# Kernel optimization log

Hardware: AMD Instinct MI355X
Metric: run time of the kernel (lower is better)

The kernel has to match this reference:

```python
import jax, jax.numpy as jnp
import numpy as np

N = 50_000       # nodes
E = 1_600_000    # edges (avg degree 32)
F_IN = 128       # input features
H = 32           # hidden channels (both GCNConv layers)
C = 16           # num classes


def setup_inputs() -> dict:
    key = jax.random.key(0)
    ks = jax.random.split(key, 6)
    x = jax.random.normal(ks[0], (N, F_IN), dtype=jnp.float32)
    edge_index = jax.random.randint(ks[1], (2, E), 0, N, dtype=jnp.int32)
    W1 = jax.random.normal(ks[2], (F_IN, H), dtype=jnp.float32) / np.float32(np.sqrt(F_IN))
    b1 = jnp.zeros((H,), jnp.float32)
    W2 = jax.random.normal(ks[3], (H, H), dtype=jnp.float32) / np.float32(np.sqrt(H))
    b2 = jnp.zeros((H,), jnp.float32)
    Wc = jax.random.normal(ks[4], (H, C), dtype=jnp.float32) / np.float32(np.sqrt(H))
    bc = jnp.zeros((C,), jnp.float32)
    return {"x": x, "edge_index": edge_index, "W1": W1, "b1": b1,
            "W2": W2, "b2": b2, "Wc": Wc, "bc": bc}


def _gcn_conv(x, W, b, src, dst, deg_inv_sqrt, n):
    """PyG GCNConv: xW, then D^{-1/2}(A+I)D^{-1/2} aggregation, then bias.

    src/dst already include self-loops; deg_inv_sqrt precomputed on dst.
    """
    xw = x @ W                                   # [N, H]
    norm = deg_inv_sqrt[src] * deg_inv_sqrt[dst]  # [E+N]
    msg = xw[src] * norm[:, None]                # gather + scale, [E+N, H]
    out = jax.ops.segment_sum(msg, dst, num_segments=n)  # scatter-add
    return out + b


def reference(x, edge_index, W1, b1, W2, b2, Wc, bc):
    n = x.shape[0]
    loops = jnp.arange(n, dtype=edge_index.dtype)
    src = jnp.concatenate([edge_index[0], loops])  # add self-loops
    dst = jnp.concatenate([edge_index[1], loops])
    # degree over destination column (edge weight 1), as PyG gcn_norm does
    deg = jax.ops.segment_sum(jnp.ones_like(dst, dtype=x.dtype), dst, num_segments=n)
    deg_inv_sqrt = jnp.where(deg > 0, jax.lax.rsqrt(deg), 0.0)

    h = jnp.tanh(_gcn_conv(x, W1, b1, src, dst, deg_inv_sqrt, n))
    h = jnp.tanh(_gcn_conv(h, W2, b2, src, dst, deg_inv_sqrt, n))
    out = h @ Wc + bc
    return (out, h)
```

## Files before the change

kernel.cpp:

```cpp
#include <hip/hip_runtime.h>
#include <hip/hip_bf16.h>

#define NN 50000
#define EE 1600000
#define FIN 128
#define HH 32
#define CC 16
#define NB 782
#define NBLK 391
#define CHUNK 4096

typedef unsigned short u16;
typedef unsigned int u32;
typedef unsigned char u8;

__device__ __forceinline__ float bf2f(u16 u) {
    union { u32 i; float f; } v; v.i = ((u32)u) << 16; return v.f;
}
__device__ __forceinline__ u16 f2bf(float f) {
    union { float f; u32 i; } v; v.f = f;
    u32 x = v.i;
    return (u16)((x + 0x7fffu + ((x >> 16) & 1u)) >> 16);
}

__global__ __launch_bounds__(256) void k_probe(const u32* __restrict__ xw_words, int* __restrict__ flag) {
    __shared__ int cs;
    if (threadIdx.x == 0) cs = 0;
    __syncthreads();
    int c = 0;
    for (int i = threadIdx.x; i < 512; i += 256) {
        float v = fabsf(bf2f((u16)(xw_words[i] & 0xffffu)));
        if (v >= 6.0e-8f && v <= 64.0f) c++;
    }
    atomicAdd(&cs, c);
    __syncthreads();
    if (threadIdx.x == 0) *flag = (cs > 384) ? 1 : 0;
}

__global__ __launch_bounds__(256) void k_place(const int* __restrict__ src, const int* __restrict__ dst,
                                               int* __restrict__ locT,
                                               u16* __restrict__ gsrc, u8* __restrict__ grel) {
    __shared__ int dst_s[CHUNK];
    __shared__ u16 s_src[CHUNK];
    __shared__ u8  s_rel[CHUNK];
    __shared__ int cur[NB];
    __shared__ int ps[256];
    const int tid = threadIdx.x, blk = blockIdx.x;
    const int e0 = blk * CHUNK;
    int cnt = EE - e0; if (cnt > CHUNK) cnt = CHUNK;

    const uint4* gd4 = (const uint4*)(dst + e0);
    for (int i = tid; i < cnt / 4; i += 256) ((uint4*)dst_s)[i] = gd4[i];
    for (int i = tid; i < NB; i += 256) cur[i] = 0;
    __syncthreads();

    for (int k = 0; k < CHUNK / 256; ++k) {
        int i = k * 256 + tid;
        if (i < cnt) atomicAdd(&cur[dst_s[i] >> 6], 1);
    }
    __syncthreads();

    const int bi = tid * 4;
    int v0 = 0, v1 = 0, v2 = 0, v3 = 0;
    if (bi < NB)     v0 = cur[bi];
    if (bi + 1 < NB) v1 = cur[bi + 1];
    if (bi + 2 < NB) v2 = cur[bi + 2];
    if (bi + 3 < NB) v3 = cur[bi + 3];
    ps[tid] = v0 + v1 + v2 + v3;
    __syncthreads();
    for (int off = 1; off < 256; off <<= 1) {
        int t = (tid >= off) ? ps[tid - off] : 0;
        __syncthreads();
        ps[tid] += t;
        __syncthreads();
    }
    int run = (tid == 0) ? 0 : ps[tid - 1];
    if (bi < NB)     { cur[bi] = run;     locT[(size_t)bi * NBLK + blk] = run;     run += v0; }
    if (bi + 1 < NB) { cur[bi + 1] = run; locT[(size_t)(bi + 1) * NBLK + blk] = run; run += v1; }
    if (bi + 2 < NB) { cur[bi + 2] = run; locT[(size_t)(bi + 2) * NBLK + blk] = run; run += v2; }
    if (bi + 3 < NB) { cur[bi + 3] = run; locT[(size_t)(bi + 3) * NBLK + blk] = run; run += v3; }
    if (tid == 255) locT[(size_t)NB * NBLK + blk] = ps[255];
    __syncthreads();

    for (int k = 0; k < CHUNK / 256; ++k) {
        int i = k * 256 + tid;
        if (i < cnt) {
            int d = dst_s[i];
            int pos = atomicAdd(&cur[d >> 6], 1);
            s_src[pos] = (u16)src[e0 + i];
            s_rel[pos] = (u8)(d & 63);
        }
    }
    __syncthreads();

    const uint4* ss = (const uint4*)s_src;
    uint4* gs = (uint4*)(gsrc + (size_t)blk * CHUNK);
    for (int i = tid; i < (cnt * 2) / 16; i += 256) gs[i] = ss[i];
    const uint4* sr = (const uint4*)s_rel;
    uint4* gr = (uint4*)(grel + (size_t)blk * CHUNK);
    for (int i = tid; i < cnt / 16; i += 256) gr[i] = sr[i];
}

__global__ __launch_bounds__(256) void k_btot(const int* __restrict__ locT, int* __restrict__ btot) {
    __shared__ int ps[256];
    const int cb = blockIdx.x;
    int s = 0;
    for (int b = threadIdx.x; b < NBLK; b += 256)
        s += locT[(size_t)(cb + 1) * NBLK + b] - locT[(size_t)cb * NBLK + b];
    ps[threadIdx.x] = s;
    __syncthreads();
    for (int off = 128; off > 0; off >>= 1) {
        if (threadIdx.x < off) ps[threadIdx.x] += ps[threadIdx.x + off];
        __syncthreads();
    }
    if (threadIdx.x == 0) btot[cb] = ps[0];
}

__global__ __launch_bounds__(1024) void k_cscan(const int* __restrict__ btot, int* __restrict__ cbase,
                                                int* __restrict__ rowptr) {
    __shared__ int ps[1024];
    const int t = threadIdx.x;
    int myv = (t < NB) ? btot[t] : 0;
    ps[t] = myv;
    __syncthreads();
    for (int off = 1; off < 1024; off <<= 1) {
        int v = (t >= off) ? ps[t - off] : 0;
        __syncthreads();
        ps[t] += v;
        __syncthreads();
    }
    if (t < NB) cbase[t] = ps[t] - myv;
    if (t == 0) { cbase[NB] = EE; rowptr[NN] = EE; }
}

__global__ __launch_bounds__(256) void k_fine(const int* __restrict__ locT, const int* __restrict__ cbase,
                                              const u16* __restrict__ gsrc, const u8* __restrict__ grel,
                                              int* __restrict__ rowptr, float* __restrict__ dis,
                                              u16* __restrict__ entries) {
    __shared__ int beg_s[NBLK];
    __shared__ int fo[NBLK + 1];
    __shared__ int ps[256];
    __shared__ int h[64];
    __shared__ int cur[64];
    const int tid = threadIdx.x, cb = blockIdx.x;

    for (int b = tid; b < NBLK; b += 256) {
        int beg = locT[(size_t)cb * NBLK + b];
        beg_s[b] = beg;
        fo[b] = locT[(size_t)(cb + 1) * NBLK + b] - beg;
    }
    if (tid < 64) h[tid] = 0;
    __syncthreads();

    const int b0 = tid * 2;
    int a = (b0 < NBLK) ? fo[b0] : 0;
    int b1v = (b0 + 1 < NBLK) ? fo[b0 + 1] : 0;
    ps[tid] = a + b1v;
    __syncthreads();
    for (int off = 1; off < 256; off <<= 1) {
        int v = (tid >= off) ? ps[tid - off] : 0;
        __syncthreads();
        ps[tid] += v;
        __syncthreads();
    }
    int run = (tid == 0) ? 0 : ps[tid - 1];
    if (b0 < NBLK)     { fo[b0] = run;     run += a; }
    if (b0 + 1 < NBLK) { fo[b0 + 1] = run; run += b1v; }
    if (tid == 255) fo[NBLK] = ps[255];
    __syncthreads();
    const int T = fo[NBLK];

    for (int i = tid; i < T; i += 256) {
        int lo = 0, hi = NBLK;
        while (hi - lo > 1) { int mid = (lo + hi) >> 1; if (fo[mid] <= i) lo = mid; else hi = mid; }
        int g = lo * CHUNK + beg_s[lo] + (i - fo[lo]);
        atomicAdd(&h[grel[g]], 1);
    }
    __syncthreads();

    const int node0 = cb * 64;
    const int base = cbase[cb];
    int myv = (tid < 64) ? h[tid] : 0;
    ps[tid] = (tid < 64) ? myv : 0;
    __syncthreads();
    for (int off = 1; off < 64; off <<= 1) {
        int v = (tid >= off && tid < 64) ? ps[tid - off] : 0;
        __syncthreads();
        if (tid < 64) ps[tid] += v;
        __syncthreads();
    }
    if (tid < 64) {
        int excl = ps[tid] - myv;
        int n = node0 + tid;
        cur[tid] = base + excl;
        if (n < NN) {
            rowptr[n] = base + excl;
            dis[n] = rsqrtf((float)myv + 1.0f);
        }
    }
    __syncthreads();

    for (int i = tid; i < T; i += 256) {
        int lo = 0, hi = NBLK;
        while (hi - lo > 1) { int mid = (lo + hi) >> 1; if (fo[mid] <= i) lo = mid; else hi = mid; }
        int g = lo * CHUNK + beg_s[lo] + (i - fo[lo]);
        int r = grel[g];
        int pos = atomicAdd(&cur[r], 1);
        entries[pos] = gsrc[g];
    }
}

__global__ __launch_bounds__(256) void k_xw1(const void* __restrict__ xv, const void* __restrict__ W1v,
                                             const float* __restrict__ dis,
                                             const int* __restrict__ flag, u16* __restrict__ xwb) {
    __shared__ float wsm[FIN * HH];
    __shared__ float xs[128][33];
    const int f = *flag;
    const int tid = threadIdx.x;
    if (f) {
        const u16* W1 = (const u16*)W1v;
        for (int i = tid; i < FIN * HH; i += 256) wsm[i] = bf2f(W1[i]);
    } else {
        const float* W1 = (const float*)W1v;
        for (int i = tid; i < FIN * HH; i += 256) wsm[i] = W1[i];
    }
    const int n0 = blockIdx.x * 128;
    const int ct = tid & 7, rg = tid >> 3;
    const int lr = tid >> 1, lh = tid & 1;
    int ln = n0 + lr; if (ln >= NN) ln = NN - 1;
    float acc[4][4] = {};
    for (int kc = 0; kc < FIN; kc += 32) {
        __syncthreads();
        float* dq = &xs[lr][lh * 16];
        if (f) {
            const u16* lp = (const u16*)xv + (size_t)ln * FIN + lh * 16 + kc;
            uint4 a = *(const uint4*)lp;
            uint4 b = *(const uint4*)(lp + 8);
            u32 aw[4] = {a.x, a.y, a.z, a.w}, bw[4] = {b.x, b.y, b.z, b.w};
            #pragma unroll
            for (int i = 0; i < 4; ++i) {
                dq[2*i]     = bf2f((u16)(aw[i] & 0xffffu));
                dq[2*i+1]   = bf2f((u16)(aw[i] >> 16));
                dq[8+2*i]   = bf2f((u16)(bw[i] & 0xffffu));
                dq[8+2*i+1] = bf2f((u16)(bw[i] >> 16));
            }
        } else {
            const float* lp = (const float*)xv + (size_t)ln * FIN + lh * 16 + kc;
            #pragma unroll
            for (int i = 0; i < 4; ++i) {
                float4 t = *(const float4*)(lp + 4 * i);
                dq[4*i] = t.x; dq[4*i+1] = t.y; dq[4*i+2] = t.z; dq[4*i+3] = t.w;
            }
        }
        __syncthreads();
        #pragma unroll
        for (int k = 0; k < 32; ++k) {
            float4 wv = *(const float4*)&wsm[(kc + k) * HH + ct * 4];
            #pragma unroll
            for (int j = 0; j < 4; ++j) {
                float xvv = xs[rg * 4 + j][k];
                acc[j][0] = fmaf(xvv, wv.x, acc[j][0]);
                acc[j][1] = fmaf(xvv, wv.y, acc[j][1]);
                acc[j][2] = fmaf(xvv, wv.z, acc[j][2]);
                acc[j][3] = fmaf(xvv, wv.w, acc[j][3]);
            }
        }
    }
    #pragma unroll
    for (int j = 0; j < 4; ++j) {
        int n = n0 + rg * 4 + j;
        if (n < NN) {
            float dd = dis[n];
            ushort4 o;
            o.x = f2bf(dd * acc[j][0]); o.y = f2bf(dd * acc[j][1]);
            o.z = f2bf(dd * acc[j][2]); o.w = f2bf(dd * acc[j][3]);
            *(ushort4*)&xwb[(size_t)n * HH + ct * 4] = o;
        }
    }
}

__global__ __launch_bounds__(256) void k_xw2(const u16* __restrict__ h1, const void* __restrict__ W2v,
                                             const float* __restrict__ dis,
                                             const int* __restrict__ flag, u16* __restrict__ xwb) {
    __shared__ float wsm[HH * HH];
    __shared__ float xs[128][33];
    const int f = *flag;
    const int tid = threadIdx.x;
    if (f) {
        const u16* W2 = (const u16*)W2v;
        for (int i = tid; i < HH * HH; i += 256) wsm[i] = bf2f(W2[i]);
    } else {
        const float* W2 = (const float*)W2v;
        for (int i = tid; i < HH * HH; i += 256) wsm[i] = W2[i];
    }
    const int n0 = blockIdx.x * 128;
    const int lr = tid >> 1, lh = tid & 1;
    int ln = n0 + lr; if (ln >= NN) ln = NN - 1;
    const u16* lp = h1 + (size_t)ln * HH + lh * 16;
    uint4 a = *(const uint4*)lp;
    uint4 b = *(const uint4*)(lp + 8);
    float* dq = &xs[lr][lh * 16];
    u32 aw[4] = {a.x, a.y, a.z, a.w}, bw[4] = {b.x, b.y, b.z, b.w};
    #pragma unroll
    for (int i = 0; i < 4; ++i) {
        dq[2*i]     = bf2f((u16)(aw[i] & 0xffffu));
        dq[2*i+1]   = bf2f((u16)(aw[i] >> 16));
        dq[8+2*i]   = bf2f((u16)(bw[i] & 0xffffu));
        dq[8+2*i+1] = bf2f((u16)(bw[i] >> 16));
    }
    __syncthreads();
    const int ct = tid & 7, rg = tid >> 3;
    float acc[4][4] = {};
    #pragma unroll
    for (int k = 0; k < 32; ++k) {
        float4 wv = *(const float4*)&wsm[k * HH + ct * 4];
        #pragma unroll
        for (int j = 0; j < 4; ++j) {
            float xv = xs[rg * 4 + j][k];
            acc[j][0] = fmaf(xv, wv.x, acc[j][0]);
            acc[j][1] = fmaf(xv, wv.y, acc[j][1]);
            acc[j][2] = fmaf(xv, wv.z, acc[j][2]);
            acc[j][3] = fmaf(xv, wv.w, acc[j][3]);
        }
    }
    #pragma unroll
    for (int j = 0; j < 4; ++j) {
        int n = n0 + rg * 4 + j;
        if (n < NN) {
            float dd = dis[n];
            ushort4 o;
            o.x = f2bf(dd * acc[j][0]); o.y = f2bf(dd * acc[j][1]);
            o.z = f2bf(dd * acc[j][2]); o.w = f2bf(dd * acc[j][3]);
            *(ushort4*)&xwb[(size_t)n * HH + ct * 4] = o;
        }
    }
}

__global__ __launch_bounds__(256) void k_gather(const int* __restrict__ rowptr, const u16* __restrict__ entries,
                                                const u16* __restrict__ xws, const float* __restrict__ dis,
                                                const void* __restrict__ bv, const int* __restrict__ flag,
                                                int force16, u16* __restrict__ dst16, float* __restrict__ dst32) {
    const int f = *flag;
    int g = (blockIdx.x * 256 + threadIdx.x) >> 5;
    int lane = threadIdx.x & 31;
    if (g >= NN) return;
    float bias = f ? bf2f(((const u16*)bv)[lane]) : ((const float*)bv)[lane];
    const int beg = rowptr[g], end = rowptr[g + 1];
    const float dd = dis[g];
    float acc0 = bf2f(xws[(size_t)g * HH + lane]);
    float acc1 = 0.f, acc2 = 0.f, acc3 = 0.f;
    int i = beg;
    for (; i + 4 <= end; i += 4) {
        int s0 = entries[i], s1 = entries[i + 1], s2 = entries[i + 2], s3 = entries[i + 3];
        acc0 += bf2f(xws[(size_t)s0 * HH + lane]);
        acc1 += bf2f(xws[(size_t)s1 * HH + lane]);
        acc2 += bf2f(xws[(size_t)s2 * HH + lane]);
        acc3 += bf2f(xws[(size_t)s3 * HH + lane]);
    }
    for (; i < end; ++i) {
        acc0 += bf2f(xws[(size_t)entries[i] * HH + lane]);
    }
    float v = tanhf(fmaf(dd, (acc0 + acc1) + (acc2 + acc3), bias));
    size_t idx = (size_t)g * HH + lane;
    if (force16 | f) dst16[idx] = f2bf(v);
    else             dst32[idx] = v;
}

__global__ __launch_bounds__(256) void k_cls(void* __restrict__ outbase, const void* __restrict__ Wcv,
                                             const void* __restrict__ bcv, const int* __restrict__ flag) {
    __shared__ float wsm[HH * CC];
    __shared__ float bs[CC];
    const int f = *flag;
    int tid = threadIdx.x;
    if (f) {
        const u16* Wc = (const u16*)Wcv;
        for (int i = tid; i < HH * CC; i += 256) wsm[i] = bf2f(Wc[i]);
        if (tid < CC) bs[tid] = bf2f(((const u16*)bcv)[tid]);
    } else {
        const float* Wc = (const float*)Wcv;
        for (int i = tid; i < HH * CC; i += 256) wsm[i] = Wc[i];
        if (tid < CC) bs[tid] = ((const float*)bcv)[tid];
    }
    __syncthreads();
    int t = blockIdx.x * 256 + tid;
    int n = t >> 4;
    if (n < NN) {
        int cl = t & 15;
        float acc = bs[cl];
        if (f) {
            const u16* r = (const u16*)outbase + (size_t)NN * CC + (size_t)n * HH;
            #pragma unroll
            for (int k = 0; k < HH; ++k) acc = fmaf(bf2f(r[k]), wsm[k * CC + cl], acc);
            ((u16*)outbase)[t] = f2bf(acc);
        } else {
            const float* r = (const float*)outbase + (size_t)NN * CC + (size_t)n * HH;
            #pragma unroll
            for (int k = 0; k < HH; ++k) acc = fmaf(r[k], wsm[k * CC + cl], acc);
            ((float*)outbase)[t] = acc;
        }
    }
}

extern "C" void kernel_launch(void* const* d_in, const int* in_sizes, int n_in,
                              void* d_out, int out_size, void* d_ws, size_t ws_size,
                              hipStream_t stream) {
    const void* x  = d_in[0];
    const int*  ei = (const int*)d_in[1];
    const void* W1 = d_in[2];
    const void* b1 = d_in[3];
    const void* W2 = d_in[4];
    const void* b2 = d_in[5];
    const void* Wc = d_in[6];
    const void* bc = d_in[7];
    const int* srcv = ei;
    const int* dstv = ei + EE;

    char*  ws     = (char*)d_ws;
    int*   flag   = (int*)ws;
    int*   rowptr = (int*)(ws + 4096);
    float* dis    = (float*)(ws + 208896);
    int*   cbase  = (int*)(ws + 413696);
    int*   btot   = (int*)(ws + 417792);
    int*   locT   = (int*)(ws + 421888);
    u16*   xwb    = (u16*)(ws + 1646592);
    u16*   entries= (u16*)(ws + 4846592);

    u16*   gsrc = (u16*)d_out;
    u8*    grel = (u8*)d_out + (size_t)EE * 2;

    u16*   h1    = (u16*)d_out;
    u16*   h2_16 = (u16*)d_out + (size_t)NN * CC;
    float* h2_32 = (float*)d_out + (size_t)NN * CC;

    k_probe<<<1, 256, 0, stream>>>((const u32*)x, flag);

    k_place<<<NBLK, 256, 0, stream>>>(srcv, dstv, locT, gsrc, grel);
    k_btot<<<NB, 256, 0, stream>>>(locT, btot);
    k_cscan<<<1, 1024, 0, stream>>>(btot, cbase, rowptr);
    k_fine<<<NB, 256, 0, stream>>>(locT, cbase, gsrc, grel, rowptr, dis, entries);

    k_xw1<<<(NN + 127) / 128, 256, 0, stream>>>(x, W1, dis, flag, xwb);
    k_gather<<<((NN * 32) + 255) / 256, 256, 0, stream>>>(rowptr, entries, xwb, dis, b1, flag,
                                                          1, h1, (float*)nullptr);

    k_xw2<<<(NN + 127) / 128, 256, 0, stream>>>(h1, W2, dis, flag, xwb);
    k_gather<<<((NN * 32) + 255) / 256, 256, 0, stream>>>(rowptr, entries, xwb, dis, b2, flag,
                                                          0, h2_16, h2_32);

    k_cls<<<(NN * CC + 255) / 256, 256, 0, stream>>>(d_out, Wc, bc, flag);
}
```

Measured before the change: 214.1 us.

## Fuse classifier into second gather, merge probe into scan, simplify fine bucketing

```diff
diff --git a/kernel.cpp b/kernel.cpp
--- a/kernel.cpp
+++ b/kernel.cpp
@@ -21,20 +21,6 @@
     union { float f; u32 i; } v; v.f = f;
     u32 x = v.i;
     return (u16)((x + 0x7fffu + ((x >> 16) & 1u)) >> 16);
-}
-
-__global__ __launch_bounds__(256) void k_probe(const u32* __restrict__ xw_words, int* __restrict__ flag) {
-    __shared__ int cs;
-    if (threadIdx.x == 0) cs = 0;
-    __syncthreads();
-    int c = 0;
-    for (int i = threadIdx.x; i < 512; i += 256) {
-        float v = fabsf(bf2f((u16)(xw_words[i] & 0xffffu)));
-        if (v >= 6.0e-8f && v <= 64.0f) c++;
-    }
-    atomicAdd(&cs, c);
-    __syncthreads();
-    if (threadIdx.x == 0) *flag = (cs > 384) ? 1 : 0;
 }
 
 __global__ __launch_bounds__(256) void k_place(const int* __restrict__ src, const int* __restrict__ dst,
@@ -117,9 +103,17 @@
 }
 
 __global__ __launch_bounds__(1024) void k_cscan(const int* __restrict__ btot, int* __restrict__ cbase,
-                                                int* __restrict__ rowptr) {
+                                                int* __restrict__ rowptr,
+                                                const u32* __restrict__ xw_words, int* __restrict__ flag) {
     __shared__ int ps[1024];
+    __shared__ int cs;
     const int t = threadIdx.x;
+    if (t == 0) cs = 0;
+    __syncthreads();
+    if (t < 512) {
+        float v = fabsf(bf2f((u16)(xw_words[t] & 0xffffu)));
+        if (v >= 6.0e-8f && v <= 64.0f) atomicAdd(&cs, 1);
+    }
     int myv = (t < NB) ? btot[t] : 0;
     ps[t] = myv;
     __syncthreads();
@@ -130,7 +124,10 @@
         __syncthreads();
     }
     if (t < NB) cbase[t] = ps[t] - myv;
-    if (t == 0) { cbase[NB] = EE; rowptr[NN] = EE; }
+    if (t == 0) {
+        cbase[NB] = EE; rowptr[NN] = EE;
+        *flag = (cs > 384) ? 1 : 0;
+    }
 }
 
 __global__ __launch_bounds__(256) void k_fine(const int* __restrict__ locT, const int* __restrict__ cbase,
@@ -138,7 +135,7 @@
                                               int* __restrict__ rowptr, float* __restrict__ dis,
                                               u16* __restrict__ entries) {
     __shared__ int beg_s[NBLK];
-    __shared__ int fo[NBLK + 1];
+    __shared__ int len_s[NBLK];
     __shared__ int ps[256];
     __shared__ int h[64];
     __shared__ int cur[64];
@@ -147,34 +144,15 @@
     for (int b = tid; b < NBLK; b += 256) {
         int beg = locT[(size_t)cb * NBLK + b];
         beg_s[b] = beg;
-        fo[b] = locT[(size_t)(cb + 1) * NBLK + b] - beg;
+        len_s[b] = locT[(size_t)(cb + 1) * NBLK + b] - beg;
     }
     if (tid < 64) h[tid] = 0;
     __syncthreads();
 
-    const int b0 = tid * 2;
-    int a = (b0 < NBLK) ? fo[b0] : 0;
-    int b1v = (b0 + 1 < NBLK) ? fo[b0 + 1] : 0;
-    ps[tid] = a + b1v;
-    __syncthreads();
-    for (int off = 1; off < 256; off <<= 1) {
-        int v = (tid >= off) ? ps[tid - off] : 0;
-        __syncthreads();
-        ps[tid] += v;
-        __syncthreads();
-    }
-    int run = (tid == 0) ? 0 : ps[tid - 1];
-    if (b0 < NBLK)     { fo[b0] = run;     run += a; }
-    if (b0 + 1 < NBLK) { fo[b0 + 1] = run; run += b1v; }
-    if (tid == 255) fo[NBLK] = ps[255];
-    __syncthreads();
-    const int T = fo[NBLK];
-
-    for (int i = tid; i < T; i += 256) {
-        int lo = 0, hi = NBLK;
-        while (hi - lo > 1) { int mid = (lo + hi) >> 1; if (fo[mid] <= i) lo = mid; else hi = mid; }
-        int g = lo * CHUNK + beg_s[lo] + (i - fo[lo]);
-        atomicAdd(&h[grel[g]], 1);
+    for (int b = tid; b < NBLK; b += 256) {
+        int g0 = b * CHUNK + beg_s[b];
+        int L = len_s[b];
+        for (int j = 0; j < L; ++j) atomicAdd(&h[grel[g0 + j]], 1);
     }
     __syncthreads();
 
@@ -200,13 +178,14 @@
     }
     __syncthreads();
 
-    for (int i = tid; i < T; i += 256) {
-        int lo = 0, hi = NBLK;
-        while (hi - lo > 1) { int mid = (lo + hi) >> 1; if (fo[mid] <= i) lo = mid; else hi = mid; }
-        int g = lo * CHUNK + beg_s[lo] + (i - fo[lo]);
-        int r = grel[g];
-        int pos = atomicAdd(&cur[r], 1);
-        entries[pos] = gsrc[g];
+    for (int b = tid; b < NBLK; b += 256) {
+        int g0 = b * CHUNK + beg_s[b];
+        int L = len_s[b];
+        for (int j = 0; j < L; ++j) {
+            int g = g0 + j;
+            int pos = atomicAdd(&cur[grel[g]], 1);
+            entries[pos] = gsrc[g];
+        }
     }
 }
 
@@ -339,65 +318,72 @@
 __global__ __launch_bounds__(256) void k_gather(const int* __restrict__ rowptr, const u16* __restrict__ entries,
                                                 const u16* __restrict__ xws, const float* __restrict__ dis,
                                                 const void* __restrict__ bv, const int* __restrict__ flag,
-                                                int force16, u16* __restrict__ dst16, float* __restrict__ dst32) {
+                                                int force16, u16* __restrict__ dst16, float* __restrict__ dst32,
+                                                int do_cls, const void* __restrict__ Wcv,
+                                                const void* __restrict__ bcv, void* __restrict__ outv) {
+    __shared__ float hrow[16][32];
+    __shared__ float wcs[HH * CC];
+    __shared__ float bcs[CC];
     const int f = *flag;
-    int g = (blockIdx.x * 256 + threadIdx.x) >> 5;
-    int lane = threadIdx.x & 31;
-    if (g >= NN) return;
-    float bias = f ? bf2f(((const u16*)bv)[lane]) : ((const float*)bv)[lane];
+    const int tid = threadIdx.x;
+    if (do_cls) {
+        if (f) {
+            const u16* Wc = (const u16*)Wcv;
+            for (int i = tid; i < HH * CC; i += 256) wcs[i] = bf2f(Wc[i]);
+            if (tid < CC) bcs[tid] = bf2f(((const u16*)bcv)[tid]);
+        } else {
+            const float* Wc = (const float*)Wcv;
+            for (int i = tid; i < HH * CC; i += 256) wcs[i] = Wc[i];
+            if (tid < CC) bcs[tid] = ((const float*)bcv)[tid];
+        }
+    }
+    const int nl = tid >> 4;
+    const int g = blockIdx.x * 16 + nl;
+    const int c0 = (tid & 15) * 2;
+    float b0, b1;
+    if (f) { b0 = bf2f(((const u16*)bv)[c0]); b1 = bf2f(((const u16*)bv)[c0 + 1]); }
+    else   { b0 = ((const float*)bv)[c0];     b1 = ((const float*)bv)[c0 + 1]; }
     const int beg = rowptr[g], end = rowptr[g + 1];
     const float dd = dis[g];
-    float acc0 = bf2f(xws[(size_t)g * HH + lane]);
-    float acc1 = 0.f, acc2 = 0.f, acc3 = 0.f;
+    u32 sw = *(const u32*)&xws[(size_t)g * HH + c0];
+    float aL0 = bf2f((u16)(sw & 0xffffu)), aH0 = bf2f((u16)(sw >> 16));
+    float aL1 = 0.f, aH1 = 0.f, aL2 = 0.f, aH2 = 0.f, aL3 = 0.f, aH3 = 0.f;
     int i = beg;
     for (; i + 4 <= end; i += 4) {
         int s0 = entries[i], s1 = entries[i + 1], s2 = entries[i + 2], s3 = entries[i + 3];
-        acc0 += bf2f(xws[(size_t)s0 * HH + lane]);
-        acc1 += bf2f(xws[(size_t)s1 * HH + lane]);
-        acc2 += bf2f(xws[(size_t)s2 * HH + lane]);
-        acc3 += bf2f(xws[(size_t)s3 * HH + lane]);
+        u32 w0 = *(const u32*)&xws[(size_t)s0 * HH + c0];
+        u32 w1 = *(const u32*)&xws[(size_t)s1 * HH + c0];
+        u32 w2 = *(const u32*)&xws[(size_t)s2 * HH + c0];
+        u32 w3 = *(const u32*)&xws[(size_t)s3 * HH + c0];
+        aL0 += bf2f((u16)(w0 & 0xffffu)); aH0 += bf2f((u16)(w0 >> 16));
+        aL1 += bf2f((u16)(w1 & 0xffffu)); aH1 += bf2f((u16)(w1 >> 16));
+        aL2 += bf2f((u16)(w2 & 0xffffu)); aH2 += bf2f((u16)(w2 >> 16));
+        aL3 += bf2f((u16)(w3 & 0xffffu)); aH3 += bf2f((u16)(w3 >> 16));
     }
     for (; i < end; ++i) {
-        acc0 += bf2f(xws[(size_t)entries[i] * HH + lane]);
-    }
-    float v = tanhf(fmaf(dd, (acc0 + acc1) + (acc2 + acc3), bias));
-    size_t idx = (size_t)g * HH + lane;
-    if (force16 | f) dst16[idx] = f2bf(v);
-    else             dst32[idx] = v;
-}
-
-__global__ __launch_bounds__(256) void k_cls(void* __restrict__ outbase, const void* __restrict__ Wcv,
-                                             const void* __restrict__ bcv, const int* __restrict__ flag) {
-    __shared__ float wsm[HH * CC];
-    __shared__ float bs[CC];
-    const int f = *flag;
-    int tid = threadIdx.x;
-    if (f) {
-        const u16* Wc = (const u16*)Wcv;
-        for (int i = tid; i < HH * CC; i += 256) wsm[i] = bf2f(Wc[i]);
-        if (tid < CC) bs[tid] = bf2f(((const u16*)bcv)[tid]);
+        int s = entries[i];
+        u32 w = *(const u32*)&xws[(size_t)s * HH + c0];
+        aL0 += bf2f((u16)(w & 0xffffu)); aH0 += bf2f((u16)(w >> 16));
+    }
+    float vLo = tanhf(fmaf(dd, (aL0 + aL1) + (aL2 + aL3), b0));
+    float vHi = tanhf(fmaf(dd, (aH0 + aH1) + (aH2 + aH3), b1));
+    size_t idx = (size_t)g * HH + c0;
+    if (force16 | f) {
+        u32 o = (u32)f2bf(vLo) | ((u32)f2bf(vHi) << 16);
+        *(u32*)&dst16[idx] = o;
     } else {
-        const float* Wc = (const float*)Wcv;
-        for (int i = tid; i < HH * CC; i += 256) wsm[i] = Wc[i];
-        if (tid < CC) bs[tid] = ((const float*)bcv)[tid];
-    }
-    __syncthreads();
-    int t = blockIdx.x * 256 + tid;
-    int n = t >> 4;
-    if (n < NN) {
-        int cl = t & 15;
-        float acc = bs[cl];
-        if (f) {
-            const u16* r = (const u16*)outbase + (size_t)NN * CC + (size_t)n * HH;
-            #pragma unroll
-            for (int k = 0; k < HH; ++k) acc = fmaf(bf2f(r[k]), wsm[k * CC + cl], acc);
-            ((u16*)outbase)[t] = f2bf(acc);
-        } else {
-            const float* r = (const float*)outbase + (size_t)NN * CC + (size_t)n * HH;
-            #pragma unroll
-            for (int k = 0; k < HH; ++k) acc = fmaf(r[k], wsm[k * CC + cl], acc);
-            ((float*)outbase)[t] = acc;
-        }
+        *(float2*)&dst32[idx] = make_float2(vLo, vHi);
+    }
+    if (do_cls) {
+        hrow[nl][c0] = vLo; hrow[nl][c0 + 1] = vHi;
+        __syncthreads();
+        int cl = tid & 15;
+        float acc = bcs[cl];
+        #pragma unroll
+        for (int k = 0; k < HH; ++k) acc = fmaf(hrow[nl][k], wcs[k * CC + cl], acc);
+        size_t oi = (size_t)g * CC + cl;
+        if (f) ((u16*)outv)[oi] = f2bf(acc);
+        else   ((float*)outv)[oi] = acc;
     }
 }
 
@@ -432,20 +418,18 @@
     u16*   h2_16 = (u16*)d_out + (size_t)NN * CC;
     float* h2_32 = (float*)d_out + (size_t)NN * CC;
 
-    k_probe<<<1, 256, 0, stream>>>((const u32*)x, flag);
-
     k_place<<<NBLK, 256, 0, stream>>>(srcv, dstv, locT, gsrc, grel);
     k_btot<<<NB, 256, 0, stream>>>(locT, btot);
-    k_cscan<<<1, 1024, 0, stream>>>(btot, cbase, rowptr);
+    k_cscan<<<1, 1024, 0, stream>>>(btot, cbase, rowptr, (const u32*)x, flag);
     k_fine<<<NB, 256, 0, stream>>>(locT, cbase, gsrc, grel, rowptr, dis, entries);
 
     k_xw1<<<(NN + 127) / 128, 256, 0, stream>>>(x, W1, dis, flag, xwb);
-    k_gather<<<((NN * 32) + 255) / 256, 256, 0, stream>>>(rowptr, entries, xwb, dis, b1, flag,
-                                                          1, h1, (float*)nullptr);
+    k_gather<<<NN / 16, 256, 0, stream>>>(rowptr, entries, xwb, dis, b1, flag,
+                                          1, h1, (float*)nullptr,
+                                          0, nullptr, nullptr, nullptr);
 
     k_xw2<<<(NN + 127) / 128, 256, 0, stream>>>(h1, W2, dis, flag, xwb);
-    k_gather<<<((NN * 32) + 255) / 256, 256, 0, stream>>>(rowptr, entries, xwb, dis, b2, flag,
-                                                          0, h2_16, h2_32);
-
-    k_cls<<<(NN * CC + 255) / 256, 256, 0, stream>>>(d_out, Wc, bc, flag);
-}
+    k_gather<<<NN / 16, 256, 0, stream>>>(rowptr, entries, xwb, dis, b2, flag,
+                                          0, h2_16, h2_32,
+                                          1, Wc, bc, d_out);
+}
```

Measured after the change: 193.3 us. -9.7%, faster.
